# Optimization experiments

Hardware: AMD Instinct MI355X
Metric: run time of the kernel (lower is better)

The kernel has to match this reference:

```python
import jax, jax.numpy as jnp
import numpy as np

ALPHA = 0.2  # LeakyReLU negative slope
NEG = -1e12


def setup_inputs() -> dict:
    key = jax.random.key(0)
    ks = jax.random.split(key, 7)
    B, N, Cin, F, H = 4, 2048, 256, 64, 4
    x = jax.random.normal(ks[0], (B, N, Cin), dtype=jnp.float32)
    adj = jax.random.randint(ks[1], (N, N), 0, 2, dtype=jnp.int32)
    W = jax.random.normal(ks[2], (H, Cin, F), dtype=jnp.float32) * (1.414 / np.sqrt(Cin))
    a1 = jax.random.normal(ks[3], (H, F), dtype=jnp.float32) * 0.1
    a2 = jax.random.normal(ks[4], (H, F), dtype=jnp.float32) * 0.1
    Wl = jax.random.normal(ks[5], (F, H * F), dtype=jnp.float32) * (1.0 / np.sqrt(H * F))
    bl = jax.random.normal(ks[6], (F,), dtype=jnp.float32) * 0.01
    return {"x": x, "adj": adj, "W": W, "a1": a1, "a2": a2, "Wl": Wl, "bl": bl}


def leaky(v):
    return jnp.where(v >= 0, v, ALPHA * v)


def reference(x, adj, W, a1, a2, Wl, bl):
    # Eval mode: dropout is a no-op.
    # h: [B,H,N,F] per-head projected features
    h = jnp.einsum("bnc,hcf->bhnf", x, W)
    # additive attention: e[b,h,i,j] = leaky(h_i . a1 + h_j . a2)
    f1 = jnp.einsum("bhnf,hf->bhn", h, a1)  # source term
    f2 = jnp.einsum("bhnf,hf->bhn", h, a2)  # target term
    e = leaky(f1[:, :, :, None] + f2[:, :, None, :])  # [B,H,N,N]
    e = jnp.where(adj[None, None] > 0, e, NEG)
    # NOTE: original softmaxes over dim=1 of [B,N,N], i.e. the i axis (axis=2 here)
    att = jax.nn.softmax(e, axis=2)
    hp = jnp.einsum("bhij,bhjf->bhif", att, h)  # [B,H,N,F]
    hp = jax.nn.relu(hp)  # concat=True heads
    B, H, N, F = hp.shape
    cat = hp.transpose(0, 2, 1, 3).reshape(B, N, H * F)
    out = leaky(cat @ Wl.T + bl)  # n_heads > 1 -> linear + leakyrelu
    return out
```

## Files before the change

### kernel.cpp

```cpp
#include <hip/hip_runtime.h>
#include <hip/hip_bf16.h>
#include <stdint.h>

typedef __attribute__((ext_vector_type(8))) short short8;
typedef __attribute__((ext_vector_type(4))) float f32x4;
typedef uint32_t u32;
typedef uint16_t u16;
typedef uint8_t u8;

#define LOG2E 1.4426950408889634f


__device__ __forceinline__ u16 f2bf(float f){
  union{float f; u32 u;} x; x.f = f;
  u32 r = x.u + 0x7FFFu + ((x.u >> 16) & 1u);
  return (u16)(r >> 16);
}
__device__ __forceinline__ u32 pkbf(float a, float b){
  __hip_bfloat162 h = __float22bfloat162_rn(float2{a, b});
  union{ __hip_bfloat162 h; u32 u; } cv; cv.h = h;
  return cv.u;
}
__device__ __forceinline__ float bflo(u32 cd){ union{u32 u; float f;} v; v.u = cd << 16; return v.f; }
__device__ __forceinline__ float bfhi(u32 cd){ union{u32 u; float f;} v; v.u = cd & 0xFFFF0000u; return v.f; }

__global__ __launch_bounds__(256) void k_pre(const int* __restrict__ adj,
      const float* __restrict__ W, const float* __restrict__ Wl,
      u8* __restrict__ adjb, u16* __restrict__ WT, u16* __restrict__ Wlb){
  int bid = blockIdx.x, t = threadIdx.x;
  if (bid < 2048){
    int tt = bid*256 + t;
    const int4* ap = (const int4*)(adj + (size_t)tt*8);
    int4 v0 = ap[0], v1 = ap[1];
    u32 byte = (u32)(v0.x > 0)       | ((u32)(v0.y > 0) << 1)
             | ((u32)(v0.z > 0) << 2) | ((u32)(v0.w > 0) << 3)
             | ((u32)(v1.x > 0) << 4) | ((u32)(v1.y > 0) << 5)
             | ((u32)(v1.z > 0) << 6) | ((u32)(v1.w > 0) << 7);
    adjb[tt] = (u8)byte;
    return;
  }
  int tt = (bid - 2048)*256 + t;
  for (int i = tt; i < 4*64*256; i += 16384){
    int h = i >> 14, f = (i >> 8) & 63, c = i & 255;
    WT[i] = f2bf(W[(h*256 + c)*64 + f]);
  }
  for (int i = tt; i < 64*256; i += 16384) Wlb[i] = f2bf(Wl[i]);
}

__global__ __launch_bounds__(256) void k_proj(const float* __restrict__ x,
      const u16* __restrict__ WT, const float* __restrict__ a1, const float* __restrict__ a2,
      u16* __restrict__ hT, float* __restrict__ Aarr, float* __restrict__ Barr,
      float* __restrict__ Cexp, float* __restrict__ Dexp){
  int rt = blockIdx.x;
  int cb = blockIdx.y;
  int w = threadIdx.x >> 6, l = threadIdx.x & 63;
  int rA = rt*64 + w*16 + (l & 15);
  int kg = (l >> 4) * 8;
  f32x4 acc[4] = {};
  const float* xrow = x + (size_t)rA * 256;
  #pragma unroll
  for (int ks = 0; ks < 8; ks++){
    int c = ks*32 + kg;
    float4 xa = *(const float4*)(xrow + c);
    float4 xb = *(const float4*)(xrow + c + 4);
    union{u32 w[4]; short8 v;} A;
    A.w[0] = pkbf(xa.x, xa.y); A.w[1] = pkbf(xa.z, xa.w);
    A.w[2] = pkbf(xb.x, xb.y); A.w[3] = pkbf(xb.z, xb.w);
    #pragma unroll
    for (int q = 0; q < 4; q++){
      int col = cb*64 + q*16 + (l & 15);
      short8 Bf = *(const short8*)(WT + (size_t)col*256 + c);
      acc[q] = __builtin_amdgcn_mfma_f32_16x16x32_bf16(A.v, Bf, acc[q], 0, 0, 0);
    }
  }
  int rb = rt*64 + w*16 + (l >> 4)*4;
  int b = rb >> 11, n = rb & 2047;
  #pragma unroll
  for (int q = 0; q < 4; q++){
    int fp = cb*64 + q*16 + (l & 15);
    u32 p0 = pkbf(acc[q][0], acc[q][1]);
    u32 p1 = pkbf(acc[q][2], acc[q][3]);
    u16* dst = hT + ((size_t)(b*4 + (fp >> 6))*64 + (fp & 63))*2048 + n;
    *(uint2*)dst = uint2{p0, p1};
  }
  float a1v[4], a2v[4];
  #pragma unroll
  for (int q = 0; q < 4; q++){
    a1v[q] = a1[cb*64 + q*16 + (l & 15)];
    a2v[q] = a2[cb*64 + q*16 + (l & 15)];
  }
  float s1[4], s2[4];
  #pragma unroll
  for (int r = 0; r < 4; r++){
    s1[r] = acc[0][r]*a1v[0] + acc[1][r]*a1v[1] + acc[2][r]*a1v[2] + acc[3][r]*a1v[3];
    s2[r] = acc[0][r]*a2v[0] + acc[1][r]*a2v[1] + acc[2][r]*a2v[2] + acc[3][r]*a2v[3];
  }
  #pragma unroll
  for (int m = 1; m <= 8; m <<= 1){
    #pragma unroll
    for (int r = 0; r < 4; r++){
      s1[r] += __shfl_xor(s1[r], m);
      s2[r] += __shfl_xor(s2[r], m);
    }
  }
  if ((l & 15) == 0){
    #pragma unroll
    for (int r = 0; r < 4; r++){
      int row = rb + r;
      int bb = row >> 11, nn = row & 2047;
      int o = (bb*4 + cb)*2048 + nn;
      float fa = s1[r] * LOG2E;
      Aarr[o] = __builtin_amdgcn_exp2f(fa);
      Barr[o] = __builtin_amdgcn_exp2f(0.2f*fa);
      float fb = s2[r] * LOG2E;
      Cexp[o] = __builtin_amdgcn_exp2f(fb);
      Dexp[o] = __builtin_amdgcn_exp2f(0.2f*fb);
    }
  }
}

__global__ __launch_bounds__(256) void k_colsum(const u32* __restrict__ adjw,
      const float* __restrict__ Aarr, const float* __restrict__ Barr,
      const float* __restrict__ Cexp, const float* __restrict__ Dexp,
      u32* __restrict__ CD){
  __shared__ float AL[2048], BL[2048];
  __shared__ float part[4][64];
  int jt = blockIdx.x;
  int bh = blockIdx.y;
  int t = threadIdx.x;
  int w = t >> 6, l = t & 63;
  {
    const float4* As = (const float4*)(Aarr + bh*2048);
    const float4* Bs = (const float4*)(Barr + bh*2048);
    ((float4*)AL)[t]       = As[t];
    ((float4*)AL)[t + 256] = As[t + 256];
    ((float4*)BL)[t]       = Bs[t];
    ((float4*)BL)[t + 256] = Bs[t + 256];
  }
  int j = jt*64 + l;
  float Cj = Cexp[bh*2048 + j];
  float Dj = Dexp[bh*2048 + j];
  int wi = jt*2 + (l >> 5), sh = l & 31;
  __syncthreads();
  const u32* aw = adjw + wi;
  float acc0 = 0.f, acc1 = 0.f, acc2 = 0.f, acc3 = 0.f;
  int i0 = w * 512;
  #pragma unroll 4
  for (int i = i0; i < i0 + 512; i += 4){
    u32 w0 = aw[(size_t)(i+0)*64];
    u32 w1 = aw[(size_t)(i+1)*64];
    u32 w2 = aw[(size_t)(i+2)*64];
    u32 w3 = aw[(size_t)(i+3)*64];
    float v0 = fmaxf(AL[i+0]*Cj, BL[i+0]*Dj);
    float v1 = fmaxf(AL[i+1]*Cj, BL[i+1]*Dj);
    float v2 = fmaxf(AL[i+2]*Cj, BL[i+2]*Dj);
    float v3 = fmaxf(AL[i+3]*Cj, BL[i+3]*Dj);
    acc0 = fmaf(v0, (float)((w0 >> sh) & 1u), acc0);
    acc1 = fmaf(v1, (float)((w1 >> sh) & 1u), acc1);
    acc2 = fmaf(v2, (float)((w2 >> sh) & 1u), acc2);
    acc3 = fmaf(v3, (float)((w3 >> sh) & 1u), acc3);
  }
  part[w][l] = (acc0 + acc1) + (acc2 + acc3);
  __syncthreads();
  if (t < 64){
    float D = (part[0][l] + part[1][l]) + (part[2][l] + part[3][l]);
    float inv = 1.0f / D;
    CD[bh*2048 + j] = pkbf(Cj * inv, Dj * inv);
  }
}

__global__ __launch_bounds__(512) void k_pv(const u32* __restrict__ adjw, const u16* __restrict__ hT,
      const float* __restrict__ Aarr, const float* __restrict__ Barr,
      const u32* __restrict__ CD, u16* __restrict__ cat){
  int it = blockIdx.x;
  int bh = blockIdx.y;
  int b = bh >> 2, h = bh & 3;
  int t = threadIdx.x;
  int w = t >> 6, l = t & 63;

  __shared__ u32 maskw[128*68];
  __shared__ u16 hTl[64*136];
  __shared__ u32 CDl[128];

  {
    int row = t >> 2, seg = (t & 3) * 16;
    const u32* src = adjw + (size_t)(it*128 + row)*64 + seg;
    u32* d = maskw + row*68 + seg;
    *(uint4*)(d)      = *(const uint4*)(src);
    *(uint4*)(d + 4)  = *(const uint4*)(src + 4);
    *(uint4*)(d + 8)  = *(const uint4*)(src + 8);
    *(uint4*)(d + 12) = *(const uint4*)(src + 12);
  }

  int i_l = it*128 + w*16 + (l & 15);
  float Ai = Aarr[bh*2048 + i_l];
  float Bi = Barr[bh*2048 + i_l];
  const u32* CD_row = CD + bh*2048;
  const u16* hTrow = hT + (size_t)bh * 64 * 2048;
  int kg = (l >> 4) * 8;
  f32x4 acc[4] = {};

  for (int jc = 0; jc < 2048; jc += 128){
    __syncthreads();
    {
      int f = t >> 3, seg = (t & 7) * 16;
      const u16* src = hTrow + (size_t)f*2048 + jc + seg;
      u16* d = hTl + f*136 + seg;
      *(uint4*)(d)     = *(const uint4*)(src);
      *(uint4*)(d + 8) = *(const uint4*)(src + 8);
      if (t >= 256 && t < 320){
        int t2 = t - 256;
        *(uint2*)&CDl[t2*2] = *(const uint2*)(CD_row + jc + t2*2);
      }
    }
    __syncthreads();
    #pragma unroll
    for (int ks = 0; ks < 4; ks++){
      u32 cd[8];
      *(uint4*)(cd)     = *(const uint4*)&CDl[ks*32 + kg];
      *(uint4*)(cd + 4) = *(const uint4*)&CDl[ks*32 + kg + 4];
      u32 wrd = maskw[(w*16 + (l & 15))*68 + (jc >> 5) + ks];
      float wv[8];
      #pragma unroll
      for (int e = 0; e < 8; e++){
        float ev = fmaxf(Ai*bflo(cd[e]), Bi*bfhi(cd[e]));
        wv[e] = ev * (float)((wrd >> (kg + e)) & 1u);
      }
      union{u32 w[4]; short8 v;} A;
      A.w[0] = pkbf(wv[0], wv[1]); A.w[1] = pkbf(wv[2], wv[3]);
      A.w[2] = pkbf(wv[4], wv[5]); A.w[3] = pkbf(wv[6], wv[7]);
      #pragma unroll
      for (int q = 0; q < 4; q++){
        const short8* bp = (const short8*)&hTl[(q*16 + (l & 15))*136 + ks*32 + kg];
        acc[q] = __builtin_amdgcn_mfma_f32_16x16x32_bf16(A.v, *bp, acc[q], 0, 0, 0);
      }
    }
  }
  int nb = it*128 + w*16 + (l >> 4)*4;
  #pragma unroll
  for (int q = 0; q < 4; q++){
    int f = q*16 + (l & 15);
    #pragma unroll
    for (int r = 0; r < 4; r++){
      float v = fmaxf(acc[q][r], 0.f);
      cat[((size_t)(b*2048 + nb + r))*256 + h*64 + f] = f2bf(v);
    }
  }
}

__global__ __launch_bounds__(256) void k_out(const u16* __restrict__ cat,
                       const u16* __restrict__ Wlb, const float* __restrict__ bl,
                       float* __restrict__ out){
  int rt = blockIdx.x;
  int w = threadIdx.x >> 6, l = threadIdx.x & 63;
  int rA = rt*64 + w*16 + (l & 15);
  int kg = (l >> 4) * 8;
  f32x4 acc[4] = {};
  #pragma unroll
  for (int ks = 0; ks < 8; ks++){
    int c = ks*32 + kg;
    short8 Af = *(const short8*)(cat + (size_t)rA*256 + c);
    #pragma unroll
    for (int q = 0; q < 4; q++){
      short8 Bf = *(const short8*)(Wlb + (size_t)(q*16 + (l & 15))*256 + c);
      acc[q] = __builtin_amdgcn_mfma_f32_16x16x32_bf16(Af, Bf, acc[q], 0, 0, 0);
    }
  }
  int rb = rt*64 + w*16 + (l >> 4)*4;
  #pragma unroll
  for (int q = 0; q < 4; q++){
    int o = q*16 + (l & 15);
    float bv = bl[o];
    #pragma unroll
    for (int r = 0; r < 4; r++){
      float v = acc[q][r] + bv;
      out[(size_t)(rb + r)*64 + o] = fmaxf(v, 0.2f*v);
    }
  }
}

extern "C" void kernel_launch(void* const* d_in, const int* in_sizes, int n_in,
                              void* d_out, int out_size, void* d_ws, size_t ws_size,
                              hipStream_t stream) {
  const float* x  = (const float*)d_in[0];
  const int* adj  = (const int*)d_in[1];
  const float* W  = (const float*)d_in[2];
  const float* a1 = (const float*)d_in[3];
  const float* a2 = (const float*)d_in[4];
  const float* Wl = (const float*)d_in[5];
  const float* bl = (const float*)d_in[6];
  float* out = (float*)d_out;
  char* ws = (char*)d_ws;

  u32* adjw  = (u32*)(ws + 0x000000);
  u16* hT    = (u16*)(ws + 0x080000);
  u16* cat   = (u16*)(ws + 0x480000);
  float* Aarr= (float*)(ws + 0x880000);
  float* Barr= (float*)(ws + 0x8A0000);
  float* Cexp= (float*)(ws + 0x8C0000);
  float* Dexp= (float*)(ws + 0x8E0000);
  u32* CD    = (u32*)(ws + 0x900000);
  u16* WT    = (u16*)(ws + 0x940000);
  u16* Wlb   = (u16*)(ws + 0x960000);

  k_pre<<<2112, 256, 0, stream>>>(adj, W, Wl, (u8*)adjw, WT, Wlb);
  k_proj<<<dim3(128, 4), 256, 0, stream>>>(x, WT, a1, a2, hT, Aarr, Barr, Cexp, Dexp);
  k_colsum<<<dim3(32, 16), 256, 0, stream>>>(adjw, Aarr, Barr, Cexp, Dexp, CD);
  k_pv<<<dim3(16, 16), 512, 0, stream>>>(adjw, hT, Aarr, Barr, CD, cat);
  k_out<<<128, 256, 0, stream>>>(cat, Wlb, bl, out);
}
```

Before: 84.80 us.

## Fuse pre/proj kernels, split-K PV with fp32 partials, vectorize colsum

```diff
diff --git a/kernel.cpp b/kernel.cpp
--- a/kernel.cpp
+++ b/kernel.cpp
@@ -24,36 +24,41 @@
 __device__ __forceinline__ float bflo(u32 cd){ union{u32 u; float f;} v; v.u = cd << 16; return v.f; }
 __device__ __forceinline__ float bfhi(u32 cd){ union{u32 u; float f;} v; v.u = cd & 0xFFFF0000u; return v.f; }
 
-__global__ __launch_bounds__(256) void k_pre(const int* __restrict__ adj,
-      const float* __restrict__ W, const float* __restrict__ Wl,
-      u8* __restrict__ adjb, u16* __restrict__ WT, u16* __restrict__ Wlb){
+__global__ __launch_bounds__(256) void k_front(const float* __restrict__ x,
+      const float* __restrict__ W, const float* __restrict__ a1, const float* __restrict__ a2,
+      const int* __restrict__ adj,
+      u8* __restrict__ adjb, u16* __restrict__ hT,
+      float* __restrict__ Aarr, float* __restrict__ Barr,
+      float* __restrict__ Cexp, float* __restrict__ Dexp){
   int bid = blockIdx.x, t = threadIdx.x;
-  if (bid < 2048){
-    int tt = bid*256 + t;
-    const int4* ap = (const int4*)(adj + (size_t)tt*8);
+
+  if (bid >= 512){
+    int idx = (bid - 512)*256 + t;
+    const int4* ap = (const int4*)(adj + (size_t)idx*8);
     int4 v0 = ap[0], v1 = ap[1];
-    u32 byte = (u32)(v0.x > 0)       | ((u32)(v0.y > 0) << 1)
+    u32 byte = (u32)(v0.x > 0)        | ((u32)(v0.y > 0) << 1)
              | ((u32)(v0.z > 0) << 2) | ((u32)(v0.w > 0) << 3)
              | ((u32)(v1.x > 0) << 4) | ((u32)(v1.y > 0) << 5)
              | ((u32)(v1.z > 0) << 6) | ((u32)(v1.w > 0) << 7);
-    adjb[tt] = (u8)byte;
+    adjb[idx] = (u8)byte;
     return;
   }
-  int tt = (bid - 2048)*256 + t;
-  for (int i = tt; i < 4*64*256; i += 16384){
-    int h = i >> 14, f = (i >> 8) & 63, c = i & 255;
-    WT[i] = f2bf(W[(h*256 + c)*64 + f]);
-  }
-  for (int i = tt; i < 64*256; i += 16384) Wlb[i] = f2bf(Wl[i]);
-}
-
-__global__ __launch_bounds__(256) void k_proj(const float* __restrict__ x,
-      const u16* __restrict__ WT, const float* __restrict__ a1, const float* __restrict__ a2,
-      u16* __restrict__ hT, float* __restrict__ Aarr, float* __restrict__ Barr,
-      float* __restrict__ Cexp, float* __restrict__ Dexp){
-  int rt = blockIdx.x;
-  int cb = blockIdx.y;
-  int w = threadIdx.x >> 6, l = threadIdx.x & 63;
+  __shared__ u16 WL[64*264];
+  int rt = bid & 127, cb = bid >> 7;
+  const float* Wh = W + (size_t)cb*16384;
+  #pragma unroll 4
+  for (int p = 0; p < 16; p++){
+    int idx = p*256 + t;
+    float4 wv = ((const float4*)Wh)[idx];
+    int off = idx*4; int c = off >> 6, f0 = off & 63;
+    WL[(f0+0)*264 + c] = f2bf(wv.x);
+    WL[(f0+1)*264 + c] = f2bf(wv.y);
+    WL[(f0+2)*264 + c] = f2bf(wv.z);
+    WL[(f0+3)*264 + c] = f2bf(wv.w);
+  }
+  __syncthreads();
+
+  int w = t >> 6, l = t & 63;
   int rA = rt*64 + w*16 + (l & 15);
   int kg = (l >> 4) * 8;
   f32x4 acc[4] = {};
@@ -68,8 +73,7 @@
     A.w[2] = pkbf(xb.x, xb.y); A.w[3] = pkbf(xb.z, xb.w);
     #pragma unroll
     for (int q = 0; q < 4; q++){
-      int col = cb*64 + q*16 + (l & 15);
-      short8 Bf = *(const short8*)(WT + (size_t)col*256 + c);
+      short8 Bf = *(const short8*)&WL[(q*16 + (l & 15))*264 + c];
       acc[q] = __builtin_amdgcn_mfma_f32_16x16x32_bf16(A.v, Bf, acc[q], 0, 0, 0);
     }
   }
@@ -77,10 +81,10 @@
   int b = rb >> 11, n = rb & 2047;
   #pragma unroll
   for (int q = 0; q < 4; q++){
-    int fp = cb*64 + q*16 + (l & 15);
+    int f = q*16 + (l & 15);
     u32 p0 = pkbf(acc[q][0], acc[q][1]);
     u32 p1 = pkbf(acc[q][2], acc[q][3]);
-    u16* dst = hT + ((size_t)(b*4 + (fp >> 6))*64 + (fp & 63))*2048 + n;
+    u16* dst = hT + ((size_t)(b*4 + cb)*64 + f)*2048 + n;
     *(uint2*)dst = uint2{p0, p1};
   }
   float a1v[4], a2v[4];
@@ -140,27 +144,30 @@
   int j = jt*64 + l;
   float Cj = Cexp[bh*2048 + j];
   float Dj = Dexp[bh*2048 + j];
-  int wi = jt*2 + (l >> 5), sh = l & 31;
+  int wi = jt*2 + (l >> 5);
+  int shl = 31 - (l & 31);
   __syncthreads();
   const u32* aw = adjw + wi;
-  float acc0 = 0.f, acc1 = 0.f, acc2 = 0.f, acc3 = 0.f;
+  float acc0 = 0.f, acc1 = 0.f;
   int i0 = w * 512;
-  #pragma unroll 4
-  for (int i = i0; i < i0 + 512; i += 4){
-    u32 w0 = aw[(size_t)(i+0)*64];
-    u32 w1 = aw[(size_t)(i+1)*64];
-    u32 w2 = aw[(size_t)(i+2)*64];
-    u32 w3 = aw[(size_t)(i+3)*64];
-    float v0 = fmaxf(AL[i+0]*Cj, BL[i+0]*Dj);
-    float v1 = fmaxf(AL[i+1]*Cj, BL[i+1]*Dj);
-    float v2 = fmaxf(AL[i+2]*Cj, BL[i+2]*Dj);
-    float v3 = fmaxf(AL[i+3]*Cj, BL[i+3]*Dj);
-    acc0 = fmaf(v0, (float)((w0 >> sh) & 1u), acc0);
-    acc1 = fmaf(v1, (float)((w1 >> sh) & 1u), acc1);
-    acc2 = fmaf(v2, (float)((w2 >> sh) & 1u), acc2);
-    acc3 = fmaf(v3, (float)((w3 >> sh) & 1u), acc3);
-  }
-  part[w][l] = (acc0 + acc1) + (acc2 + acc3);
+  #pragma unroll 2
+  for (int i = i0; i < i0 + 512; i += 8){
+    float av[8], bv[8];
+    *(float4*)(av)   = *(const float4*)&AL[i];
+    *(float4*)(av+4) = *(const float4*)&AL[i+4];
+    *(float4*)(bv)   = *(const float4*)&BL[i];
+    *(float4*)(bv+4) = *(const float4*)&BL[i+4];
+    u32 m[8];
+    #pragma unroll
+    for (int k = 0; k < 8; k++) m[k] = aw[(size_t)(i+k)*64];
+    #pragma unroll
+    for (int k = 0; k < 8; k++){
+      float v = fmaxf(av[k]*Cj, bv[k]*Dj);
+      float sel = ((int)(m[k] << shl) < 0) ? v : 0.f;
+      if (k & 1) acc1 += sel; else acc0 += sel;
+    }
+  }
+  part[w][l] = acc0 + acc1;
   __syncthreads();
   if (t < 64){
     float D = (part[0][l] + part[1][l]) + (part[2][l] + part[3][l]);
@@ -169,101 +176,120 @@
   }
 }
 
-__global__ __launch_bounds__(512) void k_pv(const u32* __restrict__ adjw, const u16* __restrict__ hT,
+__global__ __launch_bounds__(256) void k_pv(const u32* __restrict__ adjw, const u16* __restrict__ hT,
       const float* __restrict__ Aarr, const float* __restrict__ Barr,
-      const u32* __restrict__ CD, u16* __restrict__ cat){
+      const u32* __restrict__ CD, float* __restrict__ part){
   int it = blockIdx.x;
   int bh = blockIdx.y;
+  int jh = blockIdx.z;
   int b = bh >> 2, h = bh & 3;
   int t = threadIdx.x;
   int w = t >> 6, l = t & 63;
 
-  __shared__ u32 maskw[128*68];
   __shared__ u16 hTl[64*136];
-  __shared__ u32 CDl[128];
-
-  {
-    int row = t >> 2, seg = (t & 3) * 16;
-    const u32* src = adjw + (size_t)(it*128 + row)*64 + seg;
-    u32* d = maskw + row*68 + seg;
-    *(uint4*)(d)      = *(const uint4*)(src);
-    *(uint4*)(d + 4)  = *(const uint4*)(src + 4);
-    *(uint4*)(d + 8)  = *(const uint4*)(src + 8);
-    *(uint4*)(d + 12) = *(const uint4*)(src + 12);
-  }
-
-  int i_l = it*128 + w*16 + (l & 15);
-  float Ai = Aarr[bh*2048 + i_l];
-  float Bi = Barr[bh*2048 + i_l];
-  const u32* CD_row = CD + bh*2048;
-  const u16* hTrow = hT + (size_t)bh * 64 * 2048;
+
+  int i0 = it*128 + w*32 + (l & 15);
+  float Ai0 = Aarr[bh*2048 + i0],      Bi0 = Barr[bh*2048 + i0];
+  float Ai1 = Aarr[bh*2048 + i0 + 16], Bi1 = Barr[bh*2048 + i0 + 16];
+  const u32* CDr = CD + bh*2048;
+  const u16* hTr = hT + (size_t)bh * 64 * 2048;
   int kg = (l >> 4) * 8;
-  f32x4 acc[4] = {};
-
-  for (int jc = 0; jc < 2048; jc += 128){
+  f32x4 acc[2][4] = {};
+
+  for (int jj = 0; jj < 1024; jj += 128){
+    int jc = jh*1024 + jj;
     __syncthreads();
     {
-      int f = t >> 3, seg = (t & 7) * 16;
-      const u16* src = hTrow + (size_t)f*2048 + jc + seg;
+      int f = t >> 2, seg = (t & 3) * 32;
+      const u16* src = hTr + (size_t)f*2048 + jc + seg;
       u16* d = hTl + f*136 + seg;
-      *(uint4*)(d)     = *(const uint4*)(src);
-      *(uint4*)(d + 8) = *(const uint4*)(src + 8);
-      if (t >= 256 && t < 320){
-        int t2 = t - 256;
-        *(uint2*)&CDl[t2*2] = *(const uint2*)(CD_row + jc + t2*2);
-      }
+      *(uint4*)(d)      = *(const uint4*)(src);
+      *(uint4*)(d + 8)  = *(const uint4*)(src + 8);
+      *(uint4*)(d + 16) = *(const uint4*)(src + 16);
+      *(uint4*)(d + 24) = *(const uint4*)(src + 24);
     }
     __syncthreads();
+    uint4 mw0 = *(const uint4*)(adjw + (size_t)i0*64 + (jc >> 5));
+    uint4 mw1 = *(const uint4*)(adjw + (size_t)(i0+16)*64 + (jc >> 5));
     #pragma unroll
     for (int ks = 0; ks < 4; ks++){
       u32 cd[8];
-      *(uint4*)(cd)     = *(const uint4*)&CDl[ks*32 + kg];
-      *(uint4*)(cd + 4) = *(const uint4*)&CDl[ks*32 + kg + 4];
-      u32 wrd = maskw[(w*16 + (l & 15))*68 + (jc >> 5) + ks];
-      float wv[8];
+      *(uint4*)(cd)     = *(const uint4*)(CDr + jc + ks*32 + kg);
+      *(uint4*)(cd + 4) = *(const uint4*)(CDr + jc + ks*32 + kg + 4);
+      u32 w0 = (&mw0.x)[ks] >> kg;
+      u32 w1 = (&mw1.x)[ks] >> kg;
+      float wv0[8], wv1[8];
       #pragma unroll
       for (int e = 0; e < 8; e++){
-        float ev = fmaxf(Ai*bflo(cd[e]), Bi*bfhi(cd[e]));
-        wv[e] = ev * (float)((wrd >> (kg + e)) & 1u);
+        float ca = bflo(cd[e]), db = bfhi(cd[e]);
+        float ev0 = fmaxf(Ai0*ca, Bi0*db);
+        float ev1 = fmaxf(Ai1*ca, Bi1*db);
+        wv0[e] = ((int)(w0 << (31-e)) < 0) ? ev0 : 0.f;
+        wv1[e] = ((int)(w1 << (31-e)) < 0) ? ev1 : 0.f;
       }
-      union{u32 w[4]; short8 v;} A;
-      A.w[0] = pkbf(wv[0], wv[1]); A.w[1] = pkbf(wv[2], wv[3]);
-      A.w[2] = pkbf(wv[4], wv[5]); A.w[3] = pkbf(wv[6], wv[7]);
+      union{u32 w[4]; short8 v;} A0, A1;
+      A0.w[0] = pkbf(wv0[0], wv0[1]); A0.w[1] = pkbf(wv0[2], wv0[3]);
+      A0.w[2] = pkbf(wv0[4], wv0[5]); A0.w[3] = pkbf(wv0[6], wv0[7]);
+      A1.w[0] = pkbf(wv1[0], wv1[1]); A1.w[1] = pkbf(wv1[2], wv1[3]);
+      A1.w[2] = pkbf(wv1[4], wv1[5]); A1.w[3] = pkbf(wv1[6], wv1[7]);
       #pragma unroll
       for (int q = 0; q < 4; q++){
-        const short8* bp = (const short8*)&hTl[(q*16 + (l & 15))*136 + ks*32 + kg];
-        acc[q] = __builtin_amdgcn_mfma_f32_16x16x32_bf16(A.v, *bp, acc[q], 0, 0, 0);
+        short8 Bf = *(const short8*)&hTl[(q*16 + (l & 15))*136 + ks*32 + kg];
+        acc[0][q] = __builtin_amdgcn_mfma_f32_16x16x32_bf16(A0.v, Bf, acc[0][q], 0, 0, 0);
+        acc[1][q] = __builtin_amdgcn_mfma_f32_16x16x32_bf16(A1.v, Bf, acc[1][q], 0, 0, 0);
       }
     }
   }
-  int nb = it*128 + w*16 + (l >> 4)*4;
-  #pragma unroll
-  for (int q = 0; q < 4; q++){
-    int f = q*16 + (l & 15);
-    #pragma unroll
-    for (int r = 0; r < 4; r++){
-      float v = fmaxf(acc[q][r], 0.f);
-      cat[((size_t)(b*2048 + nb + r))*256 + h*64 + f] = f2bf(v);
-    }
-  }
-}
-
-__global__ __launch_bounds__(256) void k_out(const u16* __restrict__ cat,
-                       const u16* __restrict__ Wlb, const float* __restrict__ bl,
+  float* pr = part + ((size_t)(jh*4 + b)*2048)*256;
+  #pragma unroll
+  for (int r = 0; r < 2; r++){
+    int nb = it*128 + w*32 + r*16 + (l >> 4)*4;
+    #pragma unroll
+    for (int q = 0; q < 4; q++){
+      int f = h*64 + q*16 + (l & 15);
+      #pragma unroll
+      for (int rr = 0; rr < 4; rr++){
+        pr[(size_t)(nb + rr)*256 + f] = acc[r][q][rr];
+      }
+    }
+  }
+}
+
+__global__ __launch_bounds__(256) void k_out(const float* __restrict__ part,
+                       const float* __restrict__ Wl, const float* __restrict__ bl,
                        float* __restrict__ out){
   int rt = blockIdx.x;
   int w = threadIdx.x >> 6, l = threadIdx.x & 63;
   int rA = rt*64 + w*16 + (l & 15);
+  int b = rA >> 11, n = rA & 2047;
+  const float* p0 = part + ((size_t)b*2048 + n)*256;
+  const float* p1 = part + ((size_t)(4 + b)*2048 + n)*256;
   int kg = (l >> 4) * 8;
   f32x4 acc[4] = {};
   #pragma unroll
   for (int ks = 0; ks < 8; ks++){
     int c = ks*32 + kg;
-    short8 Af = *(const short8*)(cat + (size_t)rA*256 + c);
+    float4 x0 = *(const float4*)(p0 + c);
+    float4 x1 = *(const float4*)(p0 + c + 4);
+    float4 y0 = *(const float4*)(p1 + c);
+    float4 y1 = *(const float4*)(p1 + c + 4);
+    float av[8];
+    av[0] = fmaxf(x0.x + y0.x, 0.f); av[1] = fmaxf(x0.y + y0.y, 0.f);
+    av[2] = fmaxf(x0.z + y0.z, 0.f); av[3] = fmaxf(x0.w + y0.w, 0.f);
+    av[4] = fmaxf(x1.x + y1.x, 0.f); av[5] = fmaxf(x1.y + y1.y, 0.f);
+    av[6] = fmaxf(x1.z + y1.z, 0.f); av[7] = fmaxf(x1.w + y1.w, 0.f);
+    union{u32 w[4]; short8 v;} A;
+    A.w[0] = pkbf(av[0], av[1]); A.w[1] = pkbf(av[2], av[3]);
+    A.w[2] = pkbf(av[4], av[5]); A.w[3] = pkbf(av[6], av[7]);
     #pragma unroll
     for (int q = 0; q < 4; q++){
-      short8 Bf = *(const short8*)(Wlb + (size_t)(q*16 + (l & 15))*256 + c);
-      acc[q] = __builtin_amdgcn_mfma_f32_16x16x32_bf16(Af, Bf, acc[q], 0, 0, 0);
+      const float* wr = Wl + (size_t)(q*16 + (l & 15))*256 + c;
+      float4 u0 = *(const float4*)(wr);
+      float4 u1 = *(const float4*)(wr + 4);
+      union{u32 w[4]; short8 v;} Bv;
+      Bv.w[0] = pkbf(u0.x, u0.y); Bv.w[1] = pkbf(u0.z, u0.w);
+      Bv.w[2] = pkbf(u1.x, u1.y); Bv.w[3] = pkbf(u1.z, u1.w);
+      acc[q] = __builtin_amdgcn_mfma_f32_16x16x32_bf16(A.v, Bv.v, acc[q], 0, 0, 0);
     }
   }
   int rb = rt*64 + w*16 + (l >> 4)*4;
@@ -292,20 +318,17 @@
   float* out = (float*)d_out;
   char* ws = (char*)d_ws;
 
-  u32* adjw  = (u32*)(ws + 0x000000);
-  u16* hT    = (u16*)(ws + 0x080000);
-  u16* cat   = (u16*)(ws + 0x480000);
-  float* Aarr= (float*)(ws + 0x880000);
-  float* Barr= (float*)(ws + 0x8A0000);
-  float* Cexp= (float*)(ws + 0x8C0000);
-  float* Dexp= (float*)(ws + 0x8E0000);
-  u32* CD    = (u32*)(ws + 0x900000);
-  u16* WT    = (u16*)(ws + 0x940000);
-  u16* Wlb   = (u16*)(ws + 0x960000);
-
-  k_pre<<<2112, 256, 0, stream>>>(adj, W, Wl, (u8*)adjw, WT, Wlb);
-  k_proj<<<dim3(128, 4), 256, 0, stream>>>(x, WT, a1, a2, hT, Aarr, Barr, Cexp, Dexp);
+  u32* adjw   = (u32*)(ws + 0x0000000);
+  u16* hT     = (u16*)(ws + 0x0080000);
+  float* part = (float*)(ws + 0x0480000);
+  float* Aarr = (float*)(ws + 0x1480000);
+  float* Barr = (float*)(ws + 0x14A0000);
+  float* Cexp = (float*)(ws + 0x14C0000);
+  float* Dexp = (float*)(ws + 0x14E0000);
+  u32* CD     = (u32*)(ws + 0x1500000);
+
+  k_front<<<2560, 256, 0, stream>>>(x, W, a1, a2, adj, (u8*)adjw, hT, Aarr, Barr, Cexp, Dexp);
   k_colsum<<<dim3(32, 16), 256, 0, stream>>>(adjw, Aarr, Barr, Cexp, Dexp, CD);
-  k_pv<<<dim3(16, 16), 512, 0, stream>>>(adjw, hT, Aarr, Barr, CD, cat);
-  k_out<<<128, 256, 0, stream>>>(cat, Wlb, bl, out);
-}
+  k_pv<<<dim3(16, 16, 2), 256, 0, stream>>>(adjw, hT, Aarr, Barr, CD, part);
+  k_out<<<128, 256, 0, stream>>>(part, Wl, bl, out);
+}
```

After: 81.18 us. -4.3%, faster.
